# Performance work log

Hardware: AMD Instinct MI355X
Metric: run time of the kernel (lower is better)

Reference implementation:

```python
import jax, jax.numpy as jnp
import numpy as np

QK_C = 64
VX_C = 128

def conv1x1(x, W, b):
    # x: [B,C,H,W], W: [O,C], b: [O] -> [B,O,H,W]
    return jnp.einsum('bchw,oc->bohw', x, W) + b[None, :, None, None]

def setup_inputs() -> dict:
    key = jax.random.key(0)
    ks = jax.random.split(key, 9)
    B, H, W = 4, 64, 64
    x = jax.random.normal(ks[0], (B, QK_C, H, W), dtype=jnp.float32)
    x_h = jax.random.normal(ks[1], (B, VX_C, H, W), dtype=jnp.float32)
    qc = QK_C // 4
    s_qk = 1.0 / np.sqrt(QK_C)
    s_v = 1.0 / np.sqrt(VX_C)
    Wq = jax.random.normal(ks[2], (qc, QK_C), dtype=jnp.float32) * s_qk
    bq = jax.random.normal(ks[3], (qc,), dtype=jnp.float32) * 0.01
    Wk = jax.random.normal(ks[4], (qc, QK_C), dtype=jnp.float32) * s_qk
    bk = jax.random.normal(ks[5], (qc,), dtype=jnp.float32) * 0.01
    Wv = jax.random.normal(ks[6], (VX_C, VX_C), dtype=jnp.float32) * s_v
    bv = jax.random.normal(ks[7], (VX_C,), dtype=jnp.float32) * 0.01
    # gamma initialized to zero in the torch module; use a small nonzero value
    # so the attention branch actually contributes to the output/gradients.
    gamma = jnp.array([0.1], dtype=jnp.float32)
    return {"x": x, "x_h": x_h, "Wq": Wq, "bq": bq, "Wk": Wk, "bk": bk,
            "Wv": Wv, "bv": bv, "gamma": gamma}

def reference(x, x_h, Wq, bq, Wk, bk, Wv, bv, gamma):
    B, C, H, W = x_h.shape
    b, c, h, w = x.shape
    N = h * w
    # 1x1-conv projections, flattened over spatial positions
    q = conv1x1(x, Wq, bq).reshape(b, -1, N)          # [B, qc, N]
    k = conv1x1(x, Wk, bk).reshape(b, -1, N)          # [B, qc, N]
    v = conv1x1(x_h, Wv, bv).reshape(B, C, H * W)     # [B, C, N]
    # energy[b, i, j] = <q[:, i], k[:, j]>
    energy = jnp.einsum('bdi,bdj->bij', q, k)          # [B, N, N]
    attention = jax.nn.softmax(energy, axis=-1)
    # out[b, c, i] = sum_j v[b, c, j] * attention[b, i, j]
    out = jnp.einsum('bcj,bij->bci', v, attention)     # [B, C, N]
    out = out.reshape(B, C, H, W)
    return gamma[0] * out + x_h
```

## Files before the change

### kernel.cpp

```cpp
#include <hip/hip_runtime.h>

#define BB 4
#define NN 4096
#define CQK 64
#define DQ 16
#define CV 128

typedef __attribute__((ext_vector_type(8))) short bf16x8;
typedef __attribute__((ext_vector_type(4))) float f32x4;
typedef __attribute__((ext_vector_type(8))) unsigned short u16x8;

__device__ __forceinline__ unsigned short f2bf(float f) {
    unsigned int u = __builtin_bit_cast(unsigned int, f);
    u += 0x7FFFu + ((u >> 16) & 1u);
    return (unsigned short)(u >> 16);
}
__device__ __forceinline__ unsigned int f2bf_pk(float lo, float hi) {
    return (unsigned int)f2bf(lo) | ((unsigned int)f2bf(hi) << 16);
}

__global__ __launch_bounds__(256, 4) void proj(
    const float* __restrict__ x,
    const float* __restrict__ Wq, const float* __restrict__ bq,
    const float* __restrict__ Wk, const float* __restrict__ bk,
    const float* __restrict__ xh,
    const float* __restrict__ Wv, const float* __restrict__ bv,
    unsigned short* __restrict__ qT, unsigned short* __restrict__ kT,
    unsigned short* __restrict__ vB)
{
    __shared__ __align__(16) float smem[8448];
    int tid = threadIdx.x;
    if (blockIdx.x < 512) {
        float* wvT = smem;
        float* xs  = smem + 4224;
        float* bvs = smem + 8320;
        int pt = blockIdx.x >> 1, h = blockIdx.x & 1;
        int i0 = pt * 64;
        int b = i0 >> 12, ib = i0 & 4095;
        int co0 = h * 64;
        if (tid < 64) bvs[tid] = bv[co0 + tid];
        int cog = tid & 31, ig = tid >> 5;
        float acc[8][2];
#pragma unroll
        for (int q = 0; q < 8; q++) { acc[q][0] = 0.f; acc[q][1] = 0.f; }

        for (int ch = 0; ch < 2; ch++) {
            for (int t = tid; t < 4096; t += 256) {
                int c = t & 63, col = t >> 6;
                wvT[c * 66 + col] = Wv[(size_t)(co0 + col) * CV + ch * 64 + c];
            }
            for (int t = tid; t < 4096; t += 256) {
                int il = t & 63, c = t >> 6;
                xs[c * 64 + il] = xh[((size_t)b * CV + ch * 64 + c) * NN + ib + il];
            }
            __syncthreads();
            for (int c = 0; c < 64; c++) {
                float2 w2 = *(const float2*)&wvT[c * 66 + cog * 2];
                float4 xa = *(const float4*)&xs[c * 64 + ig * 8];
                float4 xb = *(const float4*)&xs[c * 64 + ig * 8 + 4];
                float xv[8] = { xa.x, xa.y, xa.z, xa.w, xb.x, xb.y, xb.z, xb.w };
#pragma unroll
                for (int q = 0; q < 8; q++) {
                    acc[q][0] += xv[q] * w2.x;
                    acc[q][1] += xv[q] * w2.y;
                }
            }
            __syncthreads();
        }
        int kt = ib >> 6;
        int chunk = ig >> 2, quad = ig & 3;
#pragma unroll
        for (int cc = 0; cc < 2; cc++) {
            int co = co0 + cog * 2 + cc;
            int n = co >> 4, cl = co & 15;
            float bb = bvs[cog * 2 + cc];
            u16x8 o;
#pragma unroll
            for (int jj = 0; jj < 8; jj++) o[jj] = f2bf(acc[jj][cc] + bb);
            size_t base = ((size_t)(b * 64 + kt)) * 8192
                        + (size_t)(((chunk * 8 + n) * 64 + quad * 16 + cl)) * 8;
            *(u16x8*)(vB + base) = o;
        }
    } else {
        float* wqT = smem;
        float* wkT = smem + 1024;
        float* bqs = smem + 2048;
        float* bks = smem + 2064;
        for (int t = tid; t < 1024; t += 256) {
            int d = t & 15, c = t >> 4;
            wqT[t] = Wq[d * CQK + c];
            wkT[t] = Wk[d * CQK + c];
        }
        if (tid < DQ) { bqs[tid] = bq[tid]; bks[tid] = bk[tid]; }
        __syncthreads();

        int gidx = (blockIdx.x - 512) * 256 + tid;
        int b = gidx >> 12, i = gidx & 4095;
        float qa[DQ], ka[DQ];
#pragma unroll
        for (int d = 0; d < DQ; d++) { qa[d] = bqs[d]; ka[d] = bks[d]; }
        const float* xp = x + (size_t)b * CQK * NN + i;
        for (int c = 0; c < CQK; c++) {
            float xv = xp[(size_t)c * NN];
            const float4* wq4 = (const float4*)&wqT[c * DQ];
            const float4* wk4 = (const float4*)&wkT[c * DQ];
#pragma unroll
            for (int dd = 0; dd < 4; dd++) {
                float4 a = wq4[dd], e = wk4[dd];
                qa[dd*4+0] += a.x * xv; qa[dd*4+1] += a.y * xv;
                qa[dd*4+2] += a.z * xv; qa[dd*4+3] += a.w * xv;
                ka[dd*4+0] += e.x * xv; ka[dd*4+1] += e.y * xv;
                ka[dd*4+2] += e.z * xv; ka[dd*4+3] += e.w * xv;
            }
        }
        u16x8 q0, q1, k0, k1;
#pragma unroll
        for (int dd = 0; dd < 8; dd++) {
            q0[dd] = f2bf(qa[dd]);     q1[dd] = f2bf(qa[8 + dd]);
            k0[dd] = f2bf(ka[dd]);     k1[dd] = f2bf(ka[8 + dd]);
        }
        u16x8* qo = (u16x8*)(qT + (size_t)gidx * DQ);
        u16x8* ko = (u16x8*)(kT + (size_t)gidx * DQ);
        qo[0] = q0; qo[1] = q1;
        ko[0] = k0; ko[1] = k1;
    }
}

__global__ __launch_bounds__(256, 3) void flash_mfma(
    const unsigned short* __restrict__ qTb,
    const unsigned short* __restrict__ kTb,
    const unsigned short* __restrict__ vB,
    const float* __restrict__ xh,
    const float* __restrict__ gamma,
    float* __restrict__ out)
{
    __shared__ __align__(16) unsigned short pT[4 * 16 * 72];
    __shared__ __align__(16) float accs[4 * 128 * 20];
    __shared__ float l_s[4 * 64];

    int tid = threadIdx.x;
    int w = tid >> 6, lane = tid & 63;
    int quad = lane >> 4, cl = lane & 15;
    int b = blockIdx.x >> 8;
    int i0 = (blockIdx.x & 255) * 16;
    const f32x4 zf = {0.f, 0.f, 0.f, 0.f};

    bf16x8 qa = (bf16x8)(short)0;
    if (quad < 2)
        qa = *(const bf16x8*)(qTb + ((size_t)(b * NN + i0 + cl)) * DQ + quad * 8);
    int kqoff = (quad & 1) * 8;

    f32x4 acc[8];
#pragma unroll
    for (int n = 0; n < 8; n++) acc[n] = zf;
    float l = 0.f;

    const unsigned short* vtile = vB + ((size_t)(b * 64 + w * 16)) * 8192;
    const unsigned short* kbase = kTb + ((size_t)(b * NN + w * 16 * 64)) * DQ;
    unsigned short* pTw = pT + w * 16 * 72;

    bf16x8 kb[4], vb[16];
#pragma unroll
    for (int n = 0; n < 4; n++)
        kb[n] = *(const bf16x8*)(kbase + (size_t)(n * 16 + cl) * DQ + kqoff);
#pragma unroll
    for (int i = 0; i < 16; i++)
        vb[i] = *(const bf16x8*)(vtile + (size_t)i * 512 + (size_t)lane * 8);

    for (int t = 0; t < 16; t++) {
        f32x4 s[4];
#pragma unroll
        for (int n = 0; n < 4; n++)
            s[n] = __builtin_amdgcn_mfma_f32_16x16x32_bf16(kb[n], qa, zf, 0, 0, 0);
        const unsigned short* ktn = kbase + (size_t)(((t + 1) & 15) * 64) * DQ;
#pragma unroll
        for (int n = 0; n < 4; n++)
            kb[n] = *(const bf16x8*)(ktn + (size_t)(n * 16 + cl) * DQ + kqoff);

#pragma unroll
        for (int n = 0; n < 4; n++) {
            float p0 = __expf(s[n][0]);
            float p1 = __expf(s[n][1]);
            float p2 = __expf(s[n][2]);
            float p3 = __expf(s[n][3]);
            l += (p0 + p1) + (p2 + p3);
            *(uint2*)(pTw + cl * 72 + n * 16 + quad * 4) =
                make_uint2(f2bf_pk(p0, p1), f2bf_pk(p2, p3));
        }

        const unsigned short* vtn = vtile + ((t < 15) ? 8192 : 0);
#pragma unroll
        for (int ch = 0; ch < 2; ch++) {
            bf16x8 pa = *(const bf16x8*)(pTw + cl * 72 + ch * 32 + quad * 8);
#pragma unroll
            for (int n = 0; n < 8; n++)
                acc[n] = __builtin_amdgcn_mfma_f32_16x16x32_bf16(pa, vb[ch * 8 + n], acc[n], 0, 0, 0);
#pragma unroll
            for (int n = 0; n < 8; n++)
                vb[ch * 8 + n] = *(const bf16x8*)(vtn + (size_t)(ch * 8 + n) * 512 + (size_t)lane * 8);
        }
        vtile = vtn;
    }

    float* aw = accs + w * 2560;
#pragma unroll
    for (int n = 0; n < 8; n++)
        *(f32x4*)(aw + (n * 16 + cl) * 20 + quad * 4) = acc[n];
    l_s[(w * 4 + quad) * 16 + cl] = l;
    __syncthreads();

    float gam = gamma[0];
    int q = tid & 15, cg = tid >> 4;
    float L = 0.f;
#pragma unroll
    for (int u = 0; u < 16; u++) L += l_s[u * 16 + q];
    float linv = 1.f / L;
#pragma unroll
    for (int cc = 0; cc < 8; cc++) {
        int c = cg + 16 * cc;
        float a = accs[c * 20 + q] + accs[2560 + c * 20 + q]
                + accs[5120 + c * 20 + q] + accs[7680 + c * 20 + q];
        size_t gi = ((size_t)(b * CV + c)) * NN + i0 + q;
        out[gi] = gam * a * linv + xh[gi];
    }
}

extern "C" void kernel_launch(void* const* d_in, const int* in_sizes, int n_in,
                              void* d_out, int out_size, void* d_ws, size_t ws_size,
                              hipStream_t stream)
{
    (void)in_sizes; (void)n_in; (void)out_size; (void)ws_size;
    const float* x  = (const float*)d_in[0];
    const float* xh = (const float*)d_in[1];
    const float* Wq = (const float*)d_in[2];
    const float* bq = (const float*)d_in[3];
    const float* Wk = (const float*)d_in[4];
    const float* bk = (const float*)d_in[5];
    const float* Wv = (const float*)d_in[6];
    const float* bv = (const float*)d_in[7];
    const float* gm = (const float*)d_in[8];
    float* out = (float*)d_out;

    char* ws = (char*)d_ws;
    unsigned short* qTb = (unsigned short*)ws;
    unsigned short* kTb = (unsigned short*)(ws + (512 << 10));
    unsigned short* vB  = (unsigned short*)(ws + (1 << 20));

    proj<<<576, 256, 0, stream>>>(x, Wq, bq, Wk, bk, xh, Wv, bv, qTb, kTb, vB);
    flash_mfma<<<BB * 256, 256, 0, stream>>>(qTb, kTb, vB, xh, gm, out);
}
```

Before: 139.1 us.

## Split projection kernels, shrink flash LDS reduction buffer, raise occupancy, truncate P to bf16

The fused projection kernel becomes two separate kernels, one for V and one for Q/K, so the Q/K blocks no longer reserve the large V shared-memory footprint. In the flash kernel the per-wave accumulator scratch is cut to a single 128x20 buffer, and the waves add into it one at a time with a barrier per wave. Launch bounds rise from 3 to 6 blocks per SM to exploit the smaller LDS footprint. Softmax probabilities are now packed to bf16 by truncation instead of round-to-nearest, which is cheaper but adds a slight downward bias.

```diff
diff --git a/kernel.cpp b/kernel.cpp
--- a/kernel.cpp
+++ b/kernel.cpp
@@ -15,118 +15,121 @@
     u += 0x7FFFu + ((u >> 16) & 1u);
     return (unsigned short)(u >> 16);
 }
-__device__ __forceinline__ unsigned int f2bf_pk(float lo, float hi) {
-    return (unsigned int)f2bf(lo) | ((unsigned int)f2bf(hi) << 16);
-}
-
-__global__ __launch_bounds__(256, 4) void proj(
+__device__ __forceinline__ unsigned int pk_trunc(float lo, float hi) {
+    unsigned int a = __builtin_bit_cast(unsigned int, lo);
+    unsigned int b = __builtin_bit_cast(unsigned int, hi);
+    return (a >> 16) | (b & 0xFFFF0000u);
+}
+
+__global__ __launch_bounds__(256, 4) void v_proj(
+    const float* __restrict__ xh,
+    const float* __restrict__ Wv, const float* __restrict__ bv,
+    unsigned short* __restrict__ vB)
+{
+    __shared__ __align__(16) float smem[8448];
+    float* wvT = smem;
+    float* xs  = smem + 4224;
+    float* bvs = smem + 8320;
+    int tid = threadIdx.x;
+    int pt = blockIdx.x >> 1, h = blockIdx.x & 1;
+    int i0 = pt * 64;
+    int b = i0 >> 12, ib = i0 & 4095;
+    int co0 = h * 64;
+    if (tid < 64) bvs[tid] = bv[co0 + tid];
+    int cog = tid & 31, ig = tid >> 5;
+    float acc[8][2];
+#pragma unroll
+    for (int q = 0; q < 8; q++) { acc[q][0] = 0.f; acc[q][1] = 0.f; }
+
+    for (int ch = 0; ch < 2; ch++) {
+        for (int t = tid; t < 4096; t += 256) {
+            int c = t & 63, col = t >> 6;
+            wvT[c * 66 + col] = Wv[(size_t)(co0 + col) * CV + ch * 64 + c];
+        }
+        for (int t = tid; t < 4096; t += 256) {
+            int il = t & 63, c = t >> 6;
+            xs[c * 64 + il] = xh[((size_t)b * CV + ch * 64 + c) * NN + ib + il];
+        }
+        __syncthreads();
+        for (int c = 0; c < 64; c++) {
+            float2 w2 = *(const float2*)&wvT[c * 66 + cog * 2];
+            float4 xa = *(const float4*)&xs[c * 64 + ig * 8];
+            float4 xb = *(const float4*)&xs[c * 64 + ig * 8 + 4];
+            float xv[8] = { xa.x, xa.y, xa.z, xa.w, xb.x, xb.y, xb.z, xb.w };
+#pragma unroll
+            for (int q = 0; q < 8; q++) {
+                acc[q][0] += xv[q] * w2.x;
+                acc[q][1] += xv[q] * w2.y;
+            }
+        }
+        __syncthreads();
+    }
+    int kt = ib >> 6;
+    int chunk = ig >> 2, quad = ig & 3;
+#pragma unroll
+    for (int cc = 0; cc < 2; cc++) {
+        int co = co0 + cog * 2 + cc;
+        int n = co >> 4, cl = co & 15;
+        float bb = bvs[cog * 2 + cc];
+        u16x8 o;
+#pragma unroll
+        for (int jj = 0; jj < 8; jj++) o[jj] = f2bf(acc[jj][cc] + bb);
+        size_t base = ((size_t)(b * 64 + kt)) * 8192
+                    + (size_t)(((chunk * 8 + n) * 64 + quad * 16 + cl)) * 8;
+        *(u16x8*)(vB + base) = o;
+    }
+}
+
+__global__ __launch_bounds__(256, 4) void qk_proj(
     const float* __restrict__ x,
     const float* __restrict__ Wq, const float* __restrict__ bq,
     const float* __restrict__ Wk, const float* __restrict__ bk,
-    const float* __restrict__ xh,
-    const float* __restrict__ Wv, const float* __restrict__ bv,
-    unsigned short* __restrict__ qT, unsigned short* __restrict__ kT,
-    unsigned short* __restrict__ vB)
-{
-    __shared__ __align__(16) float smem[8448];
+    unsigned short* __restrict__ qT, unsigned short* __restrict__ kT)
+{
+    __shared__ float wqT[CQK * DQ];
+    __shared__ float wkT[CQK * DQ];
+    __shared__ float bqs[DQ], bks[DQ];
     int tid = threadIdx.x;
-    if (blockIdx.x < 512) {
-        float* wvT = smem;
-        float* xs  = smem + 4224;
-        float* bvs = smem + 8320;
-        int pt = blockIdx.x >> 1, h = blockIdx.x & 1;
-        int i0 = pt * 64;
-        int b = i0 >> 12, ib = i0 & 4095;
-        int co0 = h * 64;
-        if (tid < 64) bvs[tid] = bv[co0 + tid];
-        int cog = tid & 31, ig = tid >> 5;
-        float acc[8][2];
-#pragma unroll
-        for (int q = 0; q < 8; q++) { acc[q][0] = 0.f; acc[q][1] = 0.f; }
-
-        for (int ch = 0; ch < 2; ch++) {
-            for (int t = tid; t < 4096; t += 256) {
-                int c = t & 63, col = t >> 6;
-                wvT[c * 66 + col] = Wv[(size_t)(co0 + col) * CV + ch * 64 + c];
-            }
-            for (int t = tid; t < 4096; t += 256) {
-                int il = t & 63, c = t >> 6;
-                xs[c * 64 + il] = xh[((size_t)b * CV + ch * 64 + c) * NN + ib + il];
-            }
-            __syncthreads();
-            for (int c = 0; c < 64; c++) {
-                float2 w2 = *(const float2*)&wvT[c * 66 + cog * 2];
-                float4 xa = *(const float4*)&xs[c * 64 + ig * 8];
-                float4 xb = *(const float4*)&xs[c * 64 + ig * 8 + 4];
-                float xv[8] = { xa.x, xa.y, xa.z, xa.w, xb.x, xb.y, xb.z, xb.w };
-#pragma unroll
-                for (int q = 0; q < 8; q++) {
-                    acc[q][0] += xv[q] * w2.x;
-                    acc[q][1] += xv[q] * w2.y;
-                }
-            }
-            __syncthreads();
-        }
-        int kt = ib >> 6;
-        int chunk = ig >> 2, quad = ig & 3;
-#pragma unroll
-        for (int cc = 0; cc < 2; cc++) {
-            int co = co0 + cog * 2 + cc;
-            int n = co >> 4, cl = co & 15;
-            float bb = bvs[cog * 2 + cc];
-            u16x8 o;
-#pragma unroll
-            for (int jj = 0; jj < 8; jj++) o[jj] = f2bf(acc[jj][cc] + bb);
-            size_t base = ((size_t)(b * 64 + kt)) * 8192
-                        + (size_t)(((chunk * 8 + n) * 64 + quad * 16 + cl)) * 8;
-            *(u16x8*)(vB + base) = o;
-        }
-    } else {
-        float* wqT = smem;
-        float* wkT = smem + 1024;
-        float* bqs = smem + 2048;
-        float* bks = smem + 2064;
-        for (int t = tid; t < 1024; t += 256) {
-            int d = t & 15, c = t >> 4;
-            wqT[t] = Wq[d * CQK + c];
-            wkT[t] = Wk[d * CQK + c];
-        }
-        if (tid < DQ) { bqs[tid] = bq[tid]; bks[tid] = bk[tid]; }
-        __syncthreads();
-
-        int gidx = (blockIdx.x - 512) * 256 + tid;
-        int b = gidx >> 12, i = gidx & 4095;
-        float qa[DQ], ka[DQ];
-#pragma unroll
-        for (int d = 0; d < DQ; d++) { qa[d] = bqs[d]; ka[d] = bks[d]; }
-        const float* xp = x + (size_t)b * CQK * NN + i;
-        for (int c = 0; c < CQK; c++) {
-            float xv = xp[(size_t)c * NN];
-            const float4* wq4 = (const float4*)&wqT[c * DQ];
-            const float4* wk4 = (const float4*)&wkT[c * DQ];
-#pragma unroll
-            for (int dd = 0; dd < 4; dd++) {
-                float4 a = wq4[dd], e = wk4[dd];
-                qa[dd*4+0] += a.x * xv; qa[dd*4+1] += a.y * xv;
-                qa[dd*4+2] += a.z * xv; qa[dd*4+3] += a.w * xv;
-                ka[dd*4+0] += e.x * xv; ka[dd*4+1] += e.y * xv;
-                ka[dd*4+2] += e.z * xv; ka[dd*4+3] += e.w * xv;
-            }
-        }
-        u16x8 q0, q1, k0, k1;
-#pragma unroll
-        for (int dd = 0; dd < 8; dd++) {
-            q0[dd] = f2bf(qa[dd]);     q1[dd] = f2bf(qa[8 + dd]);
-            k0[dd] = f2bf(ka[dd]);     k1[dd] = f2bf(ka[8 + dd]);
-        }
-        u16x8* qo = (u16x8*)(qT + (size_t)gidx * DQ);
-        u16x8* ko = (u16x8*)(kT + (size_t)gidx * DQ);
-        qo[0] = q0; qo[1] = q1;
-        ko[0] = k0; ko[1] = k1;
-    }
-}
-
-__global__ __launch_bounds__(256, 3) void flash_mfma(
+    for (int t = tid; t < 1024; t += 256) {
+        int d = t & 15, c = t >> 4;
+        wqT[t] = Wq[d * CQK + c];
+        wkT[t] = Wk[d * CQK + c];
+    }
+    if (tid < DQ) { bqs[tid] = bq[tid]; bks[tid] = bk[tid]; }
+    __syncthreads();
+
+    int gidx = blockIdx.x * 256 + tid;
+    int b = gidx >> 12, i = gidx & 4095;
+    float qa[DQ], ka[DQ];
+#pragma unroll
+    for (int d = 0; d < DQ; d++) { qa[d] = bqs[d]; ka[d] = bks[d]; }
+    const float* xp = x + (size_t)b * CQK * NN + i;
+    for (int c = 0; c < CQK; c++) {
+        float xv = xp[(size_t)c * NN];
+        const float4* wq4 = (const float4*)&wqT[c * DQ];
+        const float4* wk4 = (const float4*)&wkT[c * DQ];
+#pragma unroll
+        for (int dd = 0; dd < 4; dd++) {
+            float4 a = wq4[dd], e = wk4[dd];
+            qa[dd*4+0] += a.x * xv; qa[dd*4+1] += a.y * xv;
+            qa[dd*4+2] += a.z * xv; qa[dd*4+3] += a.w * xv;
+            ka[dd*4+0] += e.x * xv; ka[dd*4+1] += e.y * xv;
+            ka[dd*4+2] += e.z * xv; ka[dd*4+3] += e.w * xv;
+        }
+    }
+    u16x8 q0, q1, k0, k1;
+#pragma unroll
+    for (int dd = 0; dd < 8; dd++) {
+        q0[dd] = f2bf(qa[dd]);     q1[dd] = f2bf(qa[8 + dd]);
+        k0[dd] = f2bf(ka[dd]);     k1[dd] = f2bf(ka[8 + dd]);
+    }
+    u16x8* qo = (u16x8*)(qT + (size_t)gidx * DQ);
+    u16x8* ko = (u16x8*)(kT + (size_t)gidx * DQ);
+    qo[0] = q0; qo[1] = q1;
+    ko[0] = k0; ko[1] = k1;
+}
+
+__global__ __launch_bounds__(256, 6) void flash_mfma(
     const unsigned short* __restrict__ qTb,
     const unsigned short* __restrict__ kTb,
     const unsigned short* __restrict__ vB,
@@ -135,7 +138,7 @@
     float* __restrict__ out)
 {
     __shared__ __align__(16) unsigned short pT[4 * 16 * 72];
-    __shared__ __align__(16) float accs[4 * 128 * 20];
+    __shared__ __align__(16) float accs[128 * 20];
     __shared__ float l_s[4 * 64];
 
     int tid = threadIdx.x;
@@ -185,7 +188,7 @@
             float p3 = __expf(s[n][3]);
             l += (p0 + p1) + (p2 + p3);
             *(uint2*)(pTw + cl * 72 + n * 16 + quad * 4) =
-                make_uint2(f2bf_pk(p0, p1), f2bf_pk(p2, p3));
+                make_uint2(pk_trunc(p0, p1), pk_trunc(p2, p3));
         }
 
         const unsigned short* vtn = vtile + ((t < 15) ? 8192 : 0);
@@ -202,12 +205,21 @@
         vtile = vtn;
     }
 
-    float* aw = accs + w * 2560;
-#pragma unroll
-    for (int n = 0; n < 8; n++)
-        *(f32x4*)(aw + (n * 16 + cl) * 20 + quad * 4) = acc[n];
     l_s[(w * 4 + quad) * 16 + cl] = l;
-    __syncthreads();
+    for (int ww = 0; ww < 4; ww++) {
+        if (w == ww) {
+#pragma unroll
+            for (int n = 0; n < 8; n++) {
+                float* p = accs + (n * 16 + cl) * 20 + quad * 4;
+                if (ww == 0) *(f32x4*)p = acc[n];
+                else {
+                    f32x4 o = *(const f32x4*)p;
+                    *(f32x4*)p = o + acc[n];
+                }
+            }
+        }
+        __syncthreads();
+    }
 
     float gam = gamma[0];
     int q = tid & 15, cg = tid >> 4;
@@ -218,8 +230,7 @@
 #pragma unroll
     for (int cc = 0; cc < 8; cc++) {
         int c = cg + 16 * cc;
-        float a = accs[c * 20 + q] + accs[2560 + c * 20 + q]
-                + accs[5120 + c * 20 + q] + accs[7680 + c * 20 + q];
+        float a = accs[c * 20 + q];
         size_t gi = ((size_t)(b * CV + c)) * NN + i0 + q;
         out[gi] = gam * a * linv + xh[gi];
     }
@@ -246,6 +257,7 @@
     unsigned short* kTb = (unsigned short*)(ws + (512 << 10));
     unsigned short* vB  = (unsigned short*)(ws + (1 << 20));
 
-    proj<<<576, 256, 0, stream>>>(x, Wq, bq, Wk, bk, xh, Wv, bv, qTb, kTb, vB);
+    v_proj<<<512, 256, 0, stream>>>(xh, Wv, bv, vB);
+    qk_proj<<<64, 256, 0, stream>>>(x, Wq, bq, Wk, bk, qTb, kTb);
     flash_mfma<<<BB * 256, 256, 0, stream>>>(qTb, kTb, vB, xh, gm, out);
 }
```

Result: slower. 416.5 us (+199.5%).

## Process 32 queries per block with 32x32 MFMA scores and reuse V fragments

Applied to the files above, without the earlier changes.

The flash kernel now handles 32 query rows per block instead of 16, which halves the grid. Scores are computed with 32x32x16 MFMAs, removing the zero-padded half of the 16x16x32 query operand. Each loaded V fragment now feeds two accumulator sets, doubling reuse of V loads and halving V traffic per query. The cost is more registers (launch bounds lowered to 2), a serialized per-wave reduction through a smaller shared buffer, P converted to bf16 by truncation rather than rounding, and a coalesced transpose in proj's weight loads.

```diff
diff --git a/kernel.cpp b/kernel.cpp
--- a/kernel.cpp
+++ b/kernel.cpp
@@ -8,6 +8,7 @@
 
 typedef __attribute__((ext_vector_type(8))) short bf16x8;
 typedef __attribute__((ext_vector_type(4))) float f32x4;
+typedef __attribute__((ext_vector_type(16))) float f32x16;
 typedef __attribute__((ext_vector_type(8))) unsigned short u16x8;
 
 __device__ __forceinline__ unsigned short f2bf(float f) {
@@ -15,8 +16,10 @@
     u += 0x7FFFu + ((u >> 16) & 1u);
     return (unsigned short)(u >> 16);
 }
-__device__ __forceinline__ unsigned int f2bf_pk(float lo, float hi) {
-    return (unsigned int)f2bf(lo) | ((unsigned int)f2bf(hi) << 16);
+__device__ __forceinline__ unsigned int pk_trunc(float lo, float hi) {
+    unsigned int a = __builtin_bit_cast(unsigned int, lo);
+    unsigned int b = __builtin_bit_cast(unsigned int, hi);
+    return (a >> 16) | (b & 0xFFFF0000u);
 }
 
 __global__ __launch_bounds__(256, 4) void proj(
@@ -87,9 +90,9 @@
         float* bqs = smem + 2048;
         float* bks = smem + 2064;
         for (int t = tid; t < 1024; t += 256) {
-            int d = t & 15, c = t >> 4;
-            wqT[t] = Wq[d * CQK + c];
-            wkT[t] = Wk[d * CQK + c];
+            int c = t & 63, d = t >> 6;
+            wqT[c * 16 + d] = Wq[d * CQK + c];
+            wkT[c * 16 + d] = Wk[d * CQK + c];
         }
         if (tid < DQ) { bqs[tid] = bq[tid]; bks[tid] = bk[tid]; }
         __syncthreads();
@@ -126,7 +129,7 @@
     }
 }
 
-__global__ __launch_bounds__(256, 3) void flash_mfma(
+__global__ __launch_bounds__(256, 2) void flash_mfma(
     const unsigned short* __restrict__ qTb,
     const unsigned short* __restrict__ kTb,
     const unsigned short* __restrict__ vB,
@@ -134,67 +137,76 @@
     const float* __restrict__ gamma,
     float* __restrict__ out)
 {
-    __shared__ __align__(16) unsigned short pT[4 * 16 * 72];
-    __shared__ __align__(16) float accs[4 * 128 * 20];
-    __shared__ float l_s[4 * 64];
+    __shared__ __align__(16) unsigned short pT[4 * 32 * 76];
+    __shared__ __align__(16) float accs[128 * 36];
+    __shared__ float l_s[4 * 2 * 32];
 
     int tid = threadIdx.x;
     int w = tid >> 6, lane = tid & 63;
+    int q32 = lane & 31, half = lane >> 5;
     int quad = lane >> 4, cl = lane & 15;
-    int b = blockIdx.x >> 8;
-    int i0 = (blockIdx.x & 255) * 16;
+    int b = blockIdx.x >> 7;
+    int i0 = (blockIdx.x & 127) * 32;
     const f32x4 zf = {0.f, 0.f, 0.f, 0.f};
-
-    bf16x8 qa = (bf16x8)(short)0;
-    if (quad < 2)
-        qa = *(const bf16x8*)(qTb + ((size_t)(b * NN + i0 + cl)) * DQ + quad * 8);
-    int kqoff = (quad & 1) * 8;
-
-    f32x4 acc[8];
-#pragma unroll
-    for (int n = 0; n < 8; n++) acc[n] = zf;
+    f32x16 zf16;
+#pragma unroll
+    for (int r = 0; r < 16; r++) zf16[r] = 0.f;
+
+    bf16x8 qa = *(const bf16x8*)(qTb + ((size_t)(b * NN + i0 + q32)) * DQ + half * 8);
+
+    f32x4 acc[2][8];
+#pragma unroll
+    for (int g = 0; g < 2; g++)
+#pragma unroll
+        for (int n = 0; n < 8; n++) acc[g][n] = zf;
     float l = 0.f;
 
     const unsigned short* vtile = vB + ((size_t)(b * 64 + w * 16)) * 8192;
     const unsigned short* kbase = kTb + ((size_t)(b * NN + w * 16 * 64)) * DQ;
-    unsigned short* pTw = pT + w * 16 * 72;
-
-    bf16x8 kb[4], vb[16];
-#pragma unroll
-    for (int n = 0; n < 4; n++)
-        kb[n] = *(const bf16x8*)(kbase + (size_t)(n * 16 + cl) * DQ + kqoff);
+    unsigned short* pTw = pT + w * 32 * 76;
+
+    bf16x8 kb[2], vb[16];
+#pragma unroll
+    for (int mg = 0; mg < 2; mg++)
+        kb[mg] = *(const bf16x8*)(kbase + (size_t)(mg * 32 + q32) * DQ + half * 8);
 #pragma unroll
     for (int i = 0; i < 16; i++)
         vb[i] = *(const bf16x8*)(vtile + (size_t)i * 512 + (size_t)lane * 8);
 
     for (int t = 0; t < 16; t++) {
-        f32x4 s[4];
-#pragma unroll
-        for (int n = 0; n < 4; n++)
-            s[n] = __builtin_amdgcn_mfma_f32_16x16x32_bf16(kb[n], qa, zf, 0, 0, 0);
+        f32x16 s[2];
+        s[0] = __builtin_amdgcn_mfma_f32_32x32x16_bf16(kb[0], qa, zf16, 0, 0, 0);
+        s[1] = __builtin_amdgcn_mfma_f32_32x32x16_bf16(kb[1], qa, zf16, 0, 0, 0);
         const unsigned short* ktn = kbase + (size_t)(((t + 1) & 15) * 64) * DQ;
 #pragma unroll
-        for (int n = 0; n < 4; n++)
-            kb[n] = *(const bf16x8*)(ktn + (size_t)(n * 16 + cl) * DQ + kqoff);
-
-#pragma unroll
-        for (int n = 0; n < 4; n++) {
-            float p0 = __expf(s[n][0]);
-            float p1 = __expf(s[n][1]);
-            float p2 = __expf(s[n][2]);
-            float p3 = __expf(s[n][3]);
-            l += (p0 + p1) + (p2 + p3);
-            *(uint2*)(pTw + cl * 72 + n * 16 + quad * 4) =
-                make_uint2(f2bf_pk(p0, p1), f2bf_pk(p2, p3));
+        for (int mg = 0; mg < 2; mg++)
+            kb[mg] = *(const bf16x8*)(ktn + (size_t)(mg * 32 + q32) * DQ + half * 8);
+
+#pragma unroll
+        for (int mg = 0; mg < 2; mg++) {
+#pragma unroll
+            for (int rr = 0; rr < 4; rr++) {
+                float p0 = __expf(s[mg][rr * 4 + 0]);
+                float p1 = __expf(s[mg][rr * 4 + 1]);
+                float p2 = __expf(s[mg][rr * 4 + 2]);
+                float p3 = __expf(s[mg][rr * 4 + 3]);
+                l += (p0 + p1) + (p2 + p3);
+                int k0 = mg * 32 + rr * 8 + half * 4;
+                *(uint2*)(pTw + q32 * 76 + k0) =
+                    make_uint2(pk_trunc(p0, p1), pk_trunc(p2, p3));
+            }
         }
 
         const unsigned short* vtn = vtile + ((t < 15) ? 8192 : 0);
 #pragma unroll
         for (int ch = 0; ch < 2; ch++) {
-            bf16x8 pa = *(const bf16x8*)(pTw + cl * 72 + ch * 32 + quad * 8);
-#pragma unroll
-            for (int n = 0; n < 8; n++)
-                acc[n] = __builtin_amdgcn_mfma_f32_16x16x32_bf16(pa, vb[ch * 8 + n], acc[n], 0, 0, 0);
+            bf16x8 pa0 = *(const bf16x8*)(pTw + (size_t)cl * 76 + ch * 32 + quad * 8);
+            bf16x8 pa1 = *(const bf16x8*)(pTw + (size_t)(16 + cl) * 76 + ch * 32 + quad * 8);
+#pragma unroll
+            for (int n = 0; n < 8; n++) {
+                acc[0][n] = __builtin_amdgcn_mfma_f32_16x16x32_bf16(pa0, vb[ch * 8 + n], acc[0][n], 0, 0, 0);
+                acc[1][n] = __builtin_amdgcn_mfma_f32_16x16x32_bf16(pa1, vb[ch * 8 + n], acc[1][n], 0, 0, 0);
+            }
 #pragma unroll
             for (int n = 0; n < 8; n++)
                 vb[ch * 8 + n] = *(const bf16x8*)(vtn + (size_t)(ch * 8 + n) * 512 + (size_t)lane * 8);
@@ -202,26 +214,35 @@
         vtile = vtn;
     }
 
-    float* aw = accs + w * 2560;
-#pragma unroll
-    for (int n = 0; n < 8; n++)
-        *(f32x4*)(aw + (n * 16 + cl) * 20 + quad * 4) = acc[n];
-    l_s[(w * 4 + quad) * 16 + cl] = l;
-    __syncthreads();
+    l_s[(w * 2 + half) * 32 + q32] = l;
+    for (int ww = 0; ww < 4; ww++) {
+        if (w == ww) {
+#pragma unroll
+            for (int g = 0; g < 2; g++)
+#pragma unroll
+                for (int n = 0; n < 8; n++) {
+                    float* p = accs + (n * 16 + cl) * 36 + g * 16 + quad * 4;
+                    if (ww == 0) *(f32x4*)p = acc[g][n];
+                    else {
+                        f32x4 o = *(const f32x4*)p;
+                        *(f32x4*)p = o + acc[g][n];
+                    }
+                }
+        }
+        __syncthreads();
+    }
 
     float gam = gamma[0];
-    int q = tid & 15, cg = tid >> 4;
+    int q = tid & 31, cg = tid >> 5;
     float L = 0.f;
 #pragma unroll
-    for (int u = 0; u < 16; u++) L += l_s[u * 16 + q];
+    for (int u = 0; u < 8; u++) L += l_s[u * 32 + q];
     float linv = 1.f / L;
 #pragma unroll
-    for (int cc = 0; cc < 8; cc++) {
-        int c = cg + 16 * cc;
-        float a = accs[c * 20 + q] + accs[2560 + c * 20 + q]
-                + accs[5120 + c * 20 + q] + accs[7680 + c * 20 + q];
+    for (int cc = 0; cc < 16; cc++) {
+        int c = cg * 16 + cc;
         size_t gi = ((size_t)(b * CV + c)) * NN + i0 + q;
-        out[gi] = gam * a * linv + xh[gi];
+        out[gi] = gam * accs[c * 36 + q] * linv + xh[gi];
     }
 }
 
@@ -247,5 +268,5 @@
     unsigned short* vB  = (unsigned short*)(ws + (1 << 20));
 
     proj<<<576, 256, 0, stream>>>(x, Wq, bq, Wk, bk, xh, Wv, bv, qTb, kTb, vB);
-    flash_mfma<<<BB * 256, 256, 0, stream>>>(qTb, kTb, vB, xh, gm, out);
-}
+    flash_mfma<<<BB * 128, 256, 0, stream>>>(qTb, kTb, vB, xh, gm, out);
+}
```

New measurement: 122.7 us (median of 3 runs). 11.8% less time.
